# Kernel optimization log

Hardware: AMD Instinct MI355X
Metric: run time of the kernel (lower is better)

The kernel has to match this reference:

```python
import jax, jax.numpy as jnp
import numpy as np


def setup_inputs() -> dict:
    key = jax.random.key(0)
    ks = jax.random.split(key, 7)
    D, N = 32, 3            # directions, ambient dim
    K0, K1, K2 = 500_000, 1_500_000, 1_000_000  # verts, edges, tris
    H = 256                 # num_heights
    return {
        "dirs": jax.random.normal(ks[0], (D, N), jnp.float32),
        "v_coords": jax.random.normal(ks[1], (K0, N), jnp.float32),
        "v_weights": jax.random.uniform(ks[2], (K0,), jnp.float32),
        "edge_verts": jax.random.randint(ks[3], (K1, 2), 0, K0),
        "edge_weights": jax.random.uniform(ks[4], (K1,), jnp.float32),
        "tri_verts": jax.random.randint(ks[5], (K2, 3), 0, K0),
        "tri_weights": jax.random.uniform(ks[6], (K2,), jnp.float32),
        "num_heights": H,
    }


def reference(dirs, v_coords, v_weights, edge_verts, edge_weights,
              tri_verts, tri_weights, num_heights):
    eps = 1e-12
    h = int(num_heights)
    d = dirs.shape[0]
    # L2-normalize directions (torch F.normalize with eps clamp on the norm)
    dirs = dirs / jnp.maximum(jnp.linalg.norm(dirs, axis=1, keepdims=True), eps)

    # vertex height indices: (K0, d)
    v_norms = jnp.linalg.norm(v_coords, axis=1)
    max_height = jnp.maximum(jnp.max(v_norms), eps)
    v_heights = v_coords @ dirs.T
    v_indices = jnp.clip(
        jnp.ceil((h - 1) * (max_height + v_heights) / (2.0 * max_height)),
        0, h - 1,
    ).astype(jnp.int32)

    dir_idx = jnp.arange(d)[None, :]  # broadcast against (k_i, d) bin indices
    diff_wect = jnp.zeros((d, h), jnp.float32)
    # 0-simplices (vertices), sign +1
    diff_wect = diff_wect.at[dir_idx, v_indices].add(v_weights[:, None])
    # 1-simplices (edges), sign (-1)^1 = -1: gather + max over the 2 verts
    edge_bins = jnp.max(v_indices[edge_verts], axis=1)   # (K1, d)
    diff_wect = diff_wect.at[dir_idx, edge_bins].add(-edge_weights[:, None])
    # 2-simplices (triangles), sign (+1): gather + max over the 3 verts
    tri_bins = jnp.max(v_indices[tri_verts], axis=1)     # (K2, d)
    diff_wect = diff_wect.at[dir_idx, tri_bins].add(tri_weights[:, None])

    return jnp.cumsum(diff_wect, axis=1)  # (d, h)
```

## Files before the change

### kernel.cpp

```cpp
#include <hip/hip_runtime.h>
#include <math.h>

#define NDIR 32
#define NH   256
#define BLK  512
#define NB   1024
#define PACKB 256
#define UNIT 64
#define SCALE    2048.0f
#define INVSCALE (1.0 / 2048.0)
#define BIAS  128.5f

#define WS_DIRS 8
#define WS_BMAX 128
#define WS_TAB  512

typedef _Float16 half2v __attribute__((ext_vector_type(2)));

__device__ __forceinline__ unsigned rfl_u(unsigned x) { return __builtin_amdgcn_readfirstlane(x); }

__device__ __forceinline__ unsigned pack2(float x, float y) {
    union { half2v h; unsigned u; } c;
    c.h = half2v{(_Float16)x, (_Float16)y};
    return c.u;
}
__device__ __forceinline__ half2v upk(unsigned u) {
    union { unsigned u; half2v h; } c; c.u = u; return c.h;
}
__device__ __forceinline__ float hdot(half2v a, half2v b, float acc) {
#if __has_builtin(__builtin_amdgcn_fdot2)
    return __builtin_amdgcn_fdot2(a, b, acc, false);
#else
    return acc + (float)a.x * (float)b.x + (float)a.y * (float)b.y;
#endif
}
__device__ __forceinline__ int bin_of(float hs) {
    return (int)fminf(fmaxf(hs, 0.0f), 255.0f);
}

template <bool PACKED>
__global__ void __launch_bounds__(512) wect_prep_kernel(
    const float* __restrict__ dirs, const float* __restrict__ vc, int K0,
    int P, int part_off, float* __restrict__ ws)
{
    int tid  = blockIdx.x * blockDim.x + threadIdx.x;
    int nthr = gridDim.x * blockDim.x;
    for (int i = tid; i < P * NDIR * NH; i += nthr)
        ((int*)ws)[part_off + i] = 0;
    if (blockIdx.x == 0 && threadIdx.x >= 64 && threadIdx.x < 64 + NDIR) {
        int d = threadIdx.x - 64;
        float x = dirs[d * 3 + 0], y = dirs[d * 3 + 1], z = dirs[d * 3 + 2];
        float n = fmaxf(sqrtf(x * x + y * y + z * z), 1e-12f);
        ws[WS_DIRS + d * 3 + 0] = x / n;
        ws[WS_DIRS + d * 3 + 1] = y / n;
        ws[WS_DIRS + d * 3 + 2] = z / n;
    }
    float m = 0.0f;
    uint2* tab = (uint2*)(ws + WS_TAB);
    for (int i = tid; i < K0; i += nthr) {
        float x = vc[3 * i + 0], y = vc[3 * i + 1], z = vc[3 * i + 2];
        m = fmaxf(m, x * x + y * y + z * z);
        if (PACKED) tab[i] = make_uint2(pack2(x, y), pack2(z, 0.0f));
    }
    __shared__ float wm[8];
    #pragma unroll
    for (int off = 32; off > 0; off >>= 1)
        m = fmaxf(m, __shfl_down(m, off, 64));
    if ((threadIdx.x & 63) == 0) wm[threadIdx.x >> 6] = m;
    __syncthreads();
    if (threadIdx.x == 0) {
        float r = wm[0];
        #pragma unroll
        for (int i = 1; i < 8; ++i) r = fmaxf(r, wm[i]);
        ws[WS_BMAX + blockIdx.x] = r;
    }
}

template <bool PACKED>
__global__ void __launch_bounds__(BLK, 8) wect_hist_kernel(
    const float* __restrict__ vc, const float* __restrict__ vw,
    const int*   __restrict__ ev, const float* __restrict__ ew,
    const int*   __restrict__ tv, const float* __restrict__ tw,
    int K0, int K1, int K2, int N0, int N01, int Ntot,
    int P, int part_off, float* __restrict__ ws)
{
    __shared__ int hist[NDIR * NH];
    __shared__ int nctr;
    for (int i = threadIdx.x; i < (NDIR * NH) / 4; i += BLK)
        ((int4*)hist)[i] = make_int4(0, 0, 0, 0);

    const int wave = threadIdx.x >> 6;
    const int lane = threadIdx.x & 63;
    const int b    = blockIdx.x;
    const int nu   = (Ntot - b + NB - 1) / NB;
    if (threadIdx.x == 0) nctr = 8;

    float m = 0.0f;
    for (int i = lane; i < PACKB; i += 64) m = fmaxf(m, ws[WS_BMAX + i]);
    #pragma unroll
    for (int off = 32; off > 0; off >>= 1)
        m = fmaxf(m, __shfl_xor(m, off, 64));
    float maxh = fmaxf(sqrtf(m), 1e-12f);
    float inv  = 127.5f / maxh;

    unsigned sdxy[NDIR], sdz[NDIR];
    #pragma unroll
    for (int d = 0; d < NDIR; ++d) {
        float dx = ws[WS_DIRS + 3 * d + 0] * inv;
        float dy = ws[WS_DIRS + 3 * d + 1] * inv;
        float dz = ws[WS_DIRS + 3 * d + 2] * inv;
        sdxy[d] = rfl_u(pack2(dx, dy));
        sdz[d]  = rfl_u(pack2(dz, 0.0f));
    }
    __syncthreads();

    const uint2* tab = (const uint2*)(ws + WS_TAB);
    #define LDC(J, CXY, CZ)                                                  \
        do {                                                                 \
            if constexpr (PACKED) {                                          \
                uint2 r = tab[J];                                            \
                CXY = upk(r.x); CZ = upk(r.y);                               \
            } else {                                                         \
                float _x = vc[3 * (J) + 0], _y = vc[3 * (J) + 1], _z = vc[3 * (J) + 2]; \
                CXY = half2v{(_Float16)_x, (_Float16)_y};                    \
                CZ  = half2v{(_Float16)_z, (_Float16)0.0f};                  \
            }                                                                \
        } while (0)

    int n = wave;
    while (n < nu) {
        int nxt = 0;
        if (lane == 0) nxt = atomicAdd(&nctr, 1);
        const int u = b + n * NB;

        if (u < N0) {
            int i = u * UNIT + lane;
            int j = (i < K0) ? i : 0;
            half2v xy, z;
            LDC(j, xy, z);
            int w = (i < K0) ? __float2int_rn(vw[j] * SCALE) : 0;
            #pragma unroll
            for (int d = 0; d < NDIR; ++d) {
                half2v dxy = upk(sdxy[d]), dz = upk(sdz[d]);
                float h = hdot(xy, dxy, hdot(z, dz, BIAS));
                atomicAdd(&hist[d * NH + bin_of(h)], w);
            }
        } else if (u < N01) {
            int i = (u - N0) * UNIT + lane;
            int j = (i < K1) ? i : 0;
            int2 e = ((const int2*)ev)[j];
            half2v axy, az, bxy, bz;
            LDC(e.x, axy, az);
            LDC(e.y, bxy, bz);
            int w = (i < K1) ? -__float2int_rn(ew[j] * SCALE) : 0;
            #pragma unroll
            for (int d = 0; d < NDIR; ++d) {
                half2v dxy = upk(sdxy[d]), dz = upk(sdz[d]);
                float h = fmaxf(hdot(axy, dxy, hdot(az, dz, BIAS)),
                                hdot(bxy, dxy, hdot(bz, dz, BIAS)));
                atomicAdd(&hist[d * NH + bin_of(h)], w);
            }
        } else {
            int i = (u - N01) * UNIT + lane;
            int j = (i < K2) ? i : 0;
            int va = tv[3 * j + 0], vb = tv[3 * j + 1], vcc = tv[3 * j + 2];
            half2v axy, az, bxy, bz, cxy, cz;
            LDC(va,  axy, az);
            LDC(vb,  bxy, bz);
            LDC(vcc, cxy, cz);
            int w = (i < K2) ? __float2int_rn(tw[j] * SCALE) : 0;
            #pragma unroll
            for (int d = 0; d < NDIR; ++d) {
                half2v dxy = upk(sdxy[d]), dz = upk(sdz[d]);
                float h = fmaxf(fmaxf(hdot(axy, dxy, hdot(az, dz, BIAS)),
                                      hdot(bxy, dxy, hdot(bz, dz, BIAS))),
                                hdot(cxy, dxy, hdot(cz, dz, BIAS)));
                atomicAdd(&hist[d * NH + bin_of(h)], w);
            }
        }

        n = __shfl(nxt, 0, 64);
    }
    #undef LDC

    __syncthreads();
    int* part = (int*)ws + part_off + (blockIdx.x & (P - 1)) * (NDIR * NH);
    for (int i = threadIdx.x; i < NDIR * NH; i += BLK) {
        int v = hist[i];
        if (v != 0) atomicAdd(&part[i], v);
    }
}

__global__ void wect_reduce_kernel(const float* __restrict__ ws, int P, int part_off,
                                   float* __restrict__ out) {
    __shared__ long long s[NH];
    int d = blockIdx.x, h = threadIdx.x;
    const int* part = (const int*)ws + part_off + d * NH + h;
    long long acc = 0;
    #pragma unroll 4
    for (int p = 0; p < P; ++p)
        acc += (long long)part[p * (NDIR * NH)];
    s[h] = acc;
    __syncthreads();
    #pragma unroll
    for (int off = 1; off < NH; off <<= 1) {
        long long v = (h >= off) ? s[h - off] : 0;
        __syncthreads();
        s[h] += v;
        __syncthreads();
    }
    out[d * NH + h] = (float)((double)s[h] * INVSCALE);
}

extern "C" void kernel_launch(void* const* d_in, const int* in_sizes, int n_in,
                              void* d_out, int out_size, void* d_ws, size_t ws_size,
                              hipStream_t stream) {
    const float* dirs = (const float*)d_in[0];
    const float* vc   = (const float*)d_in[1];
    const float* vw   = (const float*)d_in[2];
    const int*   ev   = (const int*)d_in[3];
    const float* ew   = (const float*)d_in[4];
    const int*   tv   = (const int*)d_in[5];
    const float* tw   = (const float*)d_in[6];
    int K0 = in_sizes[2];
    int K1 = in_sizes[4];
    int K2 = in_sizes[6];

    float* ws  = (float*)d_ws;
    float* out = (float*)d_out;

    long long words = (long long)(ws_size / 4);

    int  part_off = WS_TAB + 2 * K0;
    bool packed   = (words - part_off) >= 8LL * NDIR * NH;
    if (!packed) part_off = WS_TAB;

    long long availP = (words - part_off) / (NDIR * NH);
    int P = 1;
    while (P * 2 <= availP && P < 16) P *= 2;

    int N0 = (K0 + UNIT - 1) / UNIT;
    int N1 = (K1 + UNIT - 1) / UNIT;
    int N2 = (K2 + UNIT - 1) / UNIT;
    int N01 = N0 + N1;
    int Ntot = N01 + N2;

    if (packed) {
        wect_prep_kernel<true><<<PACKB, 512, 0, stream>>>(dirs, vc, K0, P, part_off, ws);
        wect_hist_kernel<true><<<NB, BLK, 0, stream>>>(
            vc, vw, ev, ew, tv, tw, K0, K1, K2, N0, N01, Ntot, P, part_off, ws);
    } else {
        wect_prep_kernel<false><<<PACKB, 512, 0, stream>>>(dirs, vc, K0, P, part_off, ws);
        wect_hist_kernel<false><<<NB, BLK, 0, stream>>>(
            vc, vw, ev, ew, tv, tw, K0, K1, K2, N0, N01, Ntot, P, part_off, ws);
    }
    wect_reduce_kernel<<<NDIR, NH, 0, stream>>>(ws, P, part_off, out);
}
```

Before: 62.10 us.

## Software-pipeline index loads and vertex gathers ahead of histogram compute

Restructures the work-stealing loop into a three-stage software pipeline with two register stages (A and B). Each iteration loads simplex indices two units ahead and gathers packed vertex coordinates and weights one unit ahead while it runs the binning and LDS atomics for the current unit. The aim is to hide global-memory gather latency behind the atomic-heavy compute. In exchange it uses more registers, which may reduce occupancy. Vertices and edges now always do three gathers, with duplicate indices standing in for the missing vertices, which adds redundant loads.

```diff
diff --git a/kernel.cpp b/kernel.cpp
--- a/kernel.cpp
+++ b/kernel.cpp
@@ -115,73 +115,119 @@
     __syncthreads();
 
     const uint2* tab = (const uint2*)(ws + WS_TAB);
-    #define LDC(J, CXY, CZ)                                                  \
-        do {                                                                 \
-            if constexpr (PACKED) {                                          \
-                uint2 r = tab[J];                                            \
-                CXY = upk(r.x); CZ = upk(r.y);                               \
-            } else {                                                         \
-                float _x = vc[3 * (J) + 0], _y = vc[3 * (J) + 1], _z = vc[3 * (J) + 2]; \
-                CXY = half2v{(_Float16)_x, (_Float16)_y};                    \
-                CZ  = half2v{(_Float16)_z, (_Float16)0.0f};                  \
-            }                                                                \
+
+    int ia_A, ib_A, ic_A, ia_B, ib_B, ic_B;
+    float wf_A = 0.0f, wf_B = 0.0f;
+    half2v axy_A{}, az_A{}, bxy_A{}, bz_A{}, cxy_A{}, cz_A{};
+    half2v axy_B{}, az_B{}, bxy_B{}, bz_B{}, cxy_B{}, cz_B{};
+    ia_A = ib_A = ic_A = ia_B = ib_B = ic_B = 0;
+
+    #define STAGE_IDX(U, S)                                                   \
+        do { int u_ = (U);                                                    \
+            if (u_ < N0) {                                                    \
+                int i_ = u_ * UNIT + lane;                                    \
+                int j_ = (i_ < K0) ? i_ : 0;                                  \
+                ia_##S = j_; ib_##S = j_; ic_##S = j_;                        \
+            } else if (u_ < N01) {                                            \
+                int i_ = (u_ - N0) * UNIT + lane;                             \
+                int j_ = (i_ < K1) ? i_ : 0;                                  \
+                int2 e_ = ((const int2*)ev)[j_];                              \
+                ia_##S = e_.x; ib_##S = e_.y; ic_##S = e_.y;                  \
+            } else {                                                          \
+                int i_ = (u_ - N01) * UNIT + lane;                            \
+                int j_ = (i_ < K2) ? i_ : 0;                                  \
+                ia_##S = tv[3 * j_ + 0];                                      \
+                ib_##S = tv[3 * j_ + 1];                                      \
+                ic_##S = tv[3 * j_ + 2];                                      \
+            }                                                                 \
         } while (0)
 
-    int n = wave;
-    while (n < nu) {
-        int nxt = 0;
-        if (lane == 0) nxt = atomicAdd(&nctr, 1);
-        const int u = b + n * NB;
-
-        if (u < N0) {
-            int i = u * UNIT + lane;
-            int j = (i < K0) ? i : 0;
-            half2v xy, z;
-            LDC(j, xy, z);
-            int w = (i < K0) ? __float2int_rn(vw[j] * SCALE) : 0;
-            #pragma unroll
-            for (int d = 0; d < NDIR; ++d) {
-                half2v dxy = upk(sdxy[d]), dz = upk(sdz[d]);
-                float h = hdot(xy, dxy, hdot(z, dz, BIAS));
-                atomicAdd(&hist[d * NH + bin_of(h)], w);
-            }
-        } else if (u < N01) {
-            int i = (u - N0) * UNIT + lane;
-            int j = (i < K1) ? i : 0;
-            int2 e = ((const int2*)ev)[j];
-            half2v axy, az, bxy, bz;
-            LDC(e.x, axy, az);
-            LDC(e.y, bxy, bz);
-            int w = (i < K1) ? -__float2int_rn(ew[j] * SCALE) : 0;
-            #pragma unroll
-            for (int d = 0; d < NDIR; ++d) {
-                half2v dxy = upk(sdxy[d]), dz = upk(sdz[d]);
-                float h = fmaxf(hdot(axy, dxy, hdot(az, dz, BIAS)),
-                                hdot(bxy, dxy, hdot(bz, dz, BIAS)));
-                atomicAdd(&hist[d * NH + bin_of(h)], w);
-            }
-        } else {
-            int i = (u - N01) * UNIT + lane;
-            int j = (i < K2) ? i : 0;
-            int va = tv[3 * j + 0], vb = tv[3 * j + 1], vcc = tv[3 * j + 2];
-            half2v axy, az, bxy, bz, cxy, cz;
-            LDC(va,  axy, az);
-            LDC(vb,  bxy, bz);
-            LDC(vcc, cxy, cz);
-            int w = (i < K2) ? __float2int_rn(tw[j] * SCALE) : 0;
-            #pragma unroll
-            for (int d = 0; d < NDIR; ++d) {
-                half2v dxy = upk(sdxy[d]), dz = upk(sdz[d]);
-                float h = fmaxf(fmaxf(hdot(axy, dxy, hdot(az, dz, BIAS)),
-                                      hdot(bxy, dxy, hdot(bz, dz, BIAS))),
-                                hdot(cxy, dxy, hdot(cz, dz, BIAS)));
-                atomicAdd(&hist[d * NH + bin_of(h)], w);
-            }
-        }
-
-        n = __shfl(nxt, 0, 64);
-    }
-    #undef LDC
+    #define STAGE_GATHER(U, S)                                                \
+        do { int u_ = (U);                                                    \
+            if constexpr (PACKED) {                                           \
+                uint2 ra_ = tab[ia_##S], rb_ = tab[ib_##S], rc_ = tab[ic_##S];\
+                axy_##S = upk(ra_.x); az_##S = upk(ra_.y);                    \
+                bxy_##S = upk(rb_.x); bz_##S = upk(rb_.y);                    \
+                cxy_##S = upk(rc_.x); cz_##S = upk(rc_.y);                    \
+            } else {                                                          \
+                float ax_ = vc[3 * ia_##S], ay_ = vc[3 * ia_##S + 1], azv_ = vc[3 * ia_##S + 2]; \
+                float bx_ = vc[3 * ib_##S], by_ = vc[3 * ib_##S + 1], bzv_ = vc[3 * ib_##S + 2]; \
+                float cx_ = vc[3 * ic_##S], cy_ = vc[3 * ic_##S + 1], czv_ = vc[3 * ic_##S + 2]; \
+                axy_##S = half2v{(_Float16)ax_, (_Float16)ay_}; az_##S = half2v{(_Float16)azv_, (_Float16)0.0f}; \
+                bxy_##S = half2v{(_Float16)bx_, (_Float16)by_}; bz_##S = half2v{(_Float16)bzv_, (_Float16)0.0f}; \
+                cxy_##S = half2v{(_Float16)cx_, (_Float16)cy_}; cz_##S = half2v{(_Float16)czv_, (_Float16)0.0f}; \
+            }                                                                 \
+            if (u_ < N0) {                                                    \
+                int i_ = u_ * UNIT + lane;                                    \
+                wf_##S = (i_ < K0) ? vw[i_] : 0.0f;                           \
+            } else if (u_ < N01) {                                            \
+                int i_ = (u_ - N0) * UNIT + lane;                             \
+                wf_##S = (i_ < K1) ? -ew[i_] : 0.0f;                          \
+            } else {                                                          \
+                int i_ = (u_ - N01) * UNIT + lane;                            \
+                wf_##S = (i_ < K2) ? tw[i_] : 0.0f;                           \
+            }                                                                 \
+        } while (0)
+
+    #define STAGE_COMPUTE(U, S)                                               \
+        do { int u_ = (U);                                                    \
+            int w_ = __float2int_rn(wf_##S * SCALE);                          \
+            if (u_ < N0) {                                                    \
+                _Pragma("unroll")                                             \
+                for (int d = 0; d < NDIR; ++d) {                              \
+                    half2v dxy = upk(sdxy[d]), dz = upk(sdz[d]);              \
+                    float h = hdot(axy_##S, dxy, hdot(az_##S, dz, BIAS));     \
+                    atomicAdd(&hist[d * NH + bin_of(h)], w_);                 \
+                }                                                             \
+            } else if (u_ < N01) {                                            \
+                _Pragma("unroll")                                             \
+                for (int d = 0; d < NDIR; ++d) {                              \
+                    half2v dxy = upk(sdxy[d]), dz = upk(sdz[d]);              \
+                    float h = fmaxf(hdot(axy_##S, dxy, hdot(az_##S, dz, BIAS)), \
+                                    hdot(bxy_##S, dxy, hdot(bz_##S, dz, BIAS))); \
+                    atomicAdd(&hist[d * NH + bin_of(h)], w_);                 \
+                }                                                             \
+            } else {                                                          \
+                _Pragma("unroll")                                             \
+                for (int d = 0; d < NDIR; ++d) {                              \
+                    half2v dxy = upk(sdxy[d]), dz = upk(sdz[d]);              \
+                    float h = fmaxf(fmaxf(hdot(axy_##S, dxy, hdot(az_##S, dz, BIAS)), \
+                                          hdot(bxy_##S, dxy, hdot(bz_##S, dz, BIAS))), \
+                                    hdot(cxy_##S, dxy, hdot(cz_##S, dz, BIAS))); \
+                    atomicAdd(&hist[d * NH + bin_of(h)], w_);                 \
+                }                                                             \
+            }                                                                 \
+        } while (0)
+
+    int t = 0;
+    if (lane == 0) t = atomicAdd(&nctr, 1);
+    int n1 = __shfl(t, 0, 64);
+    if (lane == 0) t = atomicAdd(&nctr, 1);
+    int n2 = __shfl(t, 0, 64);
+    int n0 = wave, n3;
+
+    if (n0 < nu) STAGE_IDX(b + n0 * NB, A);
+    if (n1 < nu) STAGE_IDX(b + n1 * NB, B);
+    if (n0 < nu) STAGE_GATHER(b + n0 * NB, A);
+
+    while (n0 < nu) {
+        if (n2 < nu) STAGE_IDX(b + n2 * NB, A);
+        if (n1 < nu) STAGE_GATHER(b + n1 * NB, B);
+        if (lane == 0) t = atomicAdd(&nctr, 1);
+        STAGE_COMPUTE(b + n0 * NB, A);
+        n3 = __shfl(t, 0, 64);
+        n0 = n1; n1 = n2; n2 = n3;
+        if (n0 >= nu) break;
+        if (n2 < nu) STAGE_IDX(b + n2 * NB, B);
+        if (n1 < nu) STAGE_GATHER(b + n1 * NB, A);
+        if (lane == 0) t = atomicAdd(&nctr, 1);
+        STAGE_COMPUTE(b + n0 * NB, B);
+        n3 = __shfl(t, 0, 64);
+        n0 = n1; n1 = n2; n2 = n3;
+    }
+    #undef STAGE_IDX
+    #undef STAGE_GATHER
+    #undef STAGE_COMPUTE
 
     __syncthreads();
     int* part = (int*)ws + part_off + (blockIdx.x & (P - 1)) * (NDIR * NH);
```

Result: slower. 187.6 us (+202.0%).

## Software-pipeline histogram gathers with double buffering and lookahead work stealing

Applied to the files above, without the earlier changes.

Replaces the single work-stealing loop with three per-simplex-type loops. Each wave claims units two steps ahead and double-buffers vertex gathers and weights. For edges and triangles it also fetches the next unit's vertex indices one stage earlier, so the dependent coordinate gathers overlap the current unit's 32-direction LDS atomic loop. This aims to hide global gather latency, at the cost of more live registers and more code, which may lower occupancy under the launch bounds.

```diff
diff --git a/kernel.cpp b/kernel.cpp
--- a/kernel.cpp
+++ b/kernel.cpp
@@ -18,6 +18,7 @@
 typedef _Float16 half2v __attribute__((ext_vector_type(2)));
 
 __device__ __forceinline__ unsigned rfl_u(unsigned x) { return __builtin_amdgcn_readfirstlane(x); }
+__device__ __forceinline__ int      rfl_i(int x)      { return __builtin_amdgcn_readfirstlane(x); }
 
 __device__ __forceinline__ unsigned pack2(float x, float y) {
     union { half2v h; unsigned u; } c;
@@ -93,6 +94,8 @@
     const int lane = threadIdx.x & 63;
     const int b    = blockIdx.x;
     const int nu   = (Ntot - b + NB - 1) / NB;
+    const int e0   = (N0  > b) ? (N0  - b + NB - 1) / NB : 0;
+    const int e1   = (N01 > b) ? (N01 - b + NB - 1) / NB : 0;
     if (threadIdx.x == 0) nctr = 8;
 
     float m = 0.0f;
@@ -115,73 +118,149 @@
     __syncthreads();
 
     const uint2* tab = (const uint2*)(ws + WS_TAB);
-    #define LDC(J, CXY, CZ)                                                  \
-        do {                                                                 \
-            if constexpr (PACKED) {                                          \
-                uint2 r = tab[J];                                            \
-                CXY = upk(r.x); CZ = upk(r.y);                               \
-            } else {                                                         \
-                float _x = vc[3 * (J) + 0], _y = vc[3 * (J) + 1], _z = vc[3 * (J) + 2]; \
-                CXY = half2v{(_Float16)_x, (_Float16)_y};                    \
-                CZ  = half2v{(_Float16)_z, (_Float16)0.0f};                  \
-            }                                                                \
+    #define LROW(J, XY, Z)                                                    \
+        do {                                                                  \
+            if constexpr (PACKED) {                                           \
+                uint2 r_ = tab[J]; XY = upk(r_.x); Z = upk(r_.y);             \
+            } else {                                                          \
+                float x_ = vc[3 * (J)], y_ = vc[3 * (J) + 1], z_ = vc[3 * (J) + 2]; \
+                XY = half2v{(_Float16)x_, (_Float16)y_};                      \
+                Z  = half2v{(_Float16)z_, (_Float16)0.0f};                    \
+            }                                                                 \
         } while (0)
 
-    int n = wave;
-    while (n < nu) {
-        int nxt = 0;
-        if (lane == 0) nxt = atomicAdd(&nctr, 1);
-        const int u = b + n * NB;
-
-        if (u < N0) {
-            int i = u * UNIT + lane;
-            int j = (i < K0) ? i : 0;
-            half2v xy, z;
-            LDC(j, xy, z);
-            int w = (i < K0) ? __float2int_rn(vw[j] * SCALE) : 0;
-            #pragma unroll
-            for (int d = 0; d < NDIR; ++d) {
-                half2v dxy = upk(sdxy[d]), dz = upk(sdz[d]);
-                float h = hdot(xy, dxy, hdot(z, dz, BIAS));
-                atomicAdd(&hist[d * NH + bin_of(h)], w);
-            }
-        } else if (u < N01) {
-            int i = (u - N0) * UNIT + lane;
-            int j = (i < K1) ? i : 0;
-            int2 e = ((const int2*)ev)[j];
-            half2v axy, az, bxy, bz;
-            LDC(e.x, axy, az);
-            LDC(e.y, bxy, bz);
-            int w = (i < K1) ? -__float2int_rn(ew[j] * SCALE) : 0;
-            #pragma unroll
-            for (int d = 0; d < NDIR; ++d) {
-                half2v dxy = upk(sdxy[d]), dz = upk(sdz[d]);
-                float h = fmaxf(hdot(axy, dxy, hdot(az, dz, BIAS)),
-                                hdot(bxy, dxy, hdot(bz, dz, BIAS)));
-                atomicAdd(&hist[d * NH + bin_of(h)], w);
-            }
-        } else {
-            int i = (u - N01) * UNIT + lane;
-            int j = (i < K2) ? i : 0;
-            int va = tv[3 * j + 0], vb = tv[3 * j + 1], vcc = tv[3 * j + 2];
-            half2v axy, az, bxy, bz, cxy, cz;
-            LDC(va,  axy, az);
-            LDC(vb,  bxy, bz);
-            LDC(vcc, cxy, cz);
-            int w = (i < K2) ? __float2int_rn(tw[j] * SCALE) : 0;
-            #pragma unroll
-            for (int d = 0; d < NDIR; ++d) {
-                half2v dxy = upk(sdxy[d]), dz = upk(sdz[d]);
-                float h = fmaxf(fmaxf(hdot(axy, dxy, hdot(az, dz, BIAS)),
-                                      hdot(bxy, dxy, hdot(bz, dz, BIAS))),
-                                hdot(cxy, dxy, hdot(cz, dz, BIAS)));
-                atomicAdd(&hist[d * NH + bin_of(h)], w);
-            }
+    #define STEAL() do { if (lane == 0) t = atomicAdd(&nctr, 1); } while (0)
+
+    int t = 0, n0 = wave, n1, n2;
+    STEAL(); n1 = rfl_i(t);
+    STEAL(); n2 = rfl_i(t);
+
+    {
+        half2v xyA{}, zA{}, xyB{}, zB{};
+        float wA = 0.0f, wB = 0.0f;
+        #define VGATH(N, S)                                                   \
+            do { int i_ = (b + (N) * NB) * UNIT + lane;                       \
+                 int j_ = (i_ < K0) ? i_ : 0;                                 \
+                 LROW(j_, xy##S, z##S);                                       \
+                 w##S = (i_ < K0) ? vw[j_] : 0.0f; } while (0)
+        #define VCOMP(S)                                                      \
+            do { int wi_ = __float2int_rn(w##S * SCALE);                      \
+                 _Pragma("unroll")                                            \
+                 for (int d = 0; d < NDIR; ++d) {                             \
+                     half2v dxy = upk(sdxy[d]), dz = upk(sdz[d]);             \
+                     float h = hdot(xy##S, dxy, hdot(z##S, dz, BIAS));        \
+                     atomicAdd(&hist[d * NH + bin_of(h)], wi_);               \
+                 } } while (0)
+        if (n0 < e0) VGATH(n0, A);
+        while (n0 < e0) {
+            if (n1 < e0) VGATH(n1, B);
+            STEAL();
+            VCOMP(A);
+            n0 = n1; n1 = n2; n2 = rfl_i(t);
+            if (n0 >= e0) break;
+            if (n1 < e0) VGATH(n1, A);
+            STEAL();
+            VCOMP(B);
+            n0 = n1; n1 = n2; n2 = rfl_i(t);
         }
-
-        n = __shfl(nxt, 0, 64);
-    }
-    #undef LDC
+        #undef VGATH
+        #undef VCOMP
+    }
+
+    {
+        int iaA = 0, ibA = 0, iaB = 0, ibB = 0;
+        half2v axyA{}, azA{}, bxyA{}, bzA{};
+        half2v axyB{}, azB{}, bxyB{}, bzB{};
+        float wA = 0.0f, wB = 0.0f;
+        #define EIDX(N, S)                                                    \
+            do { int i_ = (b + (N) * NB - N0) * UNIT + lane;                  \
+                 int j_ = (i_ < K1) ? i_ : 0;                                 \
+                 int2 e_ = ((const int2*)ev)[j_];                             \
+                 ia##S = e_.x; ib##S = e_.y; } while (0)
+        #define EGATH(N, S)                                                   \
+            do { LROW(ia##S, axy##S, az##S);                                  \
+                 LROW(ib##S, bxy##S, bz##S);                                  \
+                 int i_ = (b + (N) * NB - N0) * UNIT + lane;                  \
+                 w##S = (i_ < K1) ? -ew[i_] : 0.0f; } while (0)
+        #define ECOMP(S)                                                      \
+            do { int wi_ = __float2int_rn(w##S * SCALE);                      \
+                 _Pragma("unroll")                                            \
+                 for (int d = 0; d < NDIR; ++d) {                             \
+                     half2v dxy = upk(sdxy[d]), dz = upk(sdz[d]);             \
+                     float h = fmaxf(hdot(axy##S, dxy, hdot(az##S, dz, BIAS)),\
+                                     hdot(bxy##S, dxy, hdot(bz##S, dz, BIAS)));\
+                     atomicAdd(&hist[d * NH + bin_of(h)], wi_);               \
+                 } } while (0)
+        if (n0 < e1) EIDX(n0, A);
+        if (n1 < e1) EIDX(n1, B);
+        if (n0 < e1) EGATH(n0, A);
+        while (n0 < e1) {
+            if (n1 < e1) EGATH(n1, B);
+            if (n2 < e1) EIDX(n2, A);
+            STEAL();
+            ECOMP(A);
+            n0 = n1; n1 = n2; n2 = rfl_i(t);
+            if (n0 >= e1) break;
+            if (n1 < e1) EGATH(n1, A);
+            if (n2 < e1) EIDX(n2, B);
+            STEAL();
+            ECOMP(B);
+            n0 = n1; n1 = n2; n2 = rfl_i(t);
+        }
+        #undef EIDX
+        #undef EGATH
+        #undef ECOMP
+    }
+
+    {
+        int iaA = 0, ibA = 0, icA = 0, iaB = 0, ibB = 0, icB = 0;
+        half2v axyA{}, azA{}, bxyA{}, bzA{}, cxyA{}, czA{};
+        half2v axyB{}, azB{}, bxyB{}, bzB{}, cxyB{}, czB{};
+        float wA = 0.0f, wB = 0.0f;
+        #define TIDX(N, S)                                                    \
+            do { int i_ = (b + (N) * NB - N01) * UNIT + lane;                 \
+                 int j_ = (i_ < K2) ? i_ : 0;                                 \
+                 ia##S = tv[3 * j_ + 0];                                      \
+                 ib##S = tv[3 * j_ + 1];                                      \
+                 ic##S = tv[3 * j_ + 2]; } while (0)
+        #define TGATH(N, S)                                                   \
+            do { LROW(ia##S, axy##S, az##S);                                  \
+                 LROW(ib##S, bxy##S, bz##S);                                  \
+                 LROW(ic##S, cxy##S, cz##S);                                  \
+                 int i_ = (b + (N) * NB - N01) * UNIT + lane;                 \
+                 w##S = (i_ < K2) ? tw[i_] : 0.0f; } while (0)
+        #define TCOMP(S)                                                      \
+            do { int wi_ = __float2int_rn(w##S * SCALE);                      \
+                 _Pragma("unroll")                                            \
+                 for (int d = 0; d < NDIR; ++d) {                             \
+                     half2v dxy = upk(sdxy[d]), dz = upk(sdz[d]);             \
+                     float h = fmaxf(fmaxf(hdot(axy##S, dxy, hdot(az##S, dz, BIAS)),  \
+                                           hdot(bxy##S, dxy, hdot(bz##S, dz, BIAS))), \
+                                     hdot(cxy##S, dxy, hdot(cz##S, dz, BIAS)));\
+                     atomicAdd(&hist[d * NH + bin_of(h)], wi_);               \
+                 } } while (0)
+        if (n0 < nu) TIDX(n0, A);
+        if (n1 < nu) TIDX(n1, B);
+        if (n0 < nu) TGATH(n0, A);
+        while (n0 < nu) {
+            if (n1 < nu) TGATH(n1, B);
+            if (n2 < nu) TIDX(n2, A);
+            STEAL();
+            TCOMP(A);
+            n0 = n1; n1 = n2; n2 = rfl_i(t);
+            if (n0 >= nu) break;
+            if (n1 < nu) TGATH(n1, A);
+            if (n2 < nu) TIDX(n2, B);
+            STEAL();
+            TCOMP(B);
+            n0 = n1; n1 = n2; n2 = rfl_i(t);
+        }
+        #undef TIDX
+        #undef TGATH
+        #undef TCOMP
+    }
+    #undef LROW
+    #undef STEAL
 
     __syncthreads();
     int* part = (int*)ws + part_off + (blockIdx.x & (P - 1)) * (NDIR * NH);
```

After: 65.93 us. +6.2%, slower.

## Replace packed fp16 dot products with fp32 FMAs and LDS-broadcast directions

Applied to the files above, without the earlier changes.

Swaps the packed-half fdot2 height computation for plain fp32 FMAs, with the scaled directions kept in a shared float4 array that wave 0 fills, instead of 64 SGPR-resident packed constants recomputed by every wave. It also clamps bins with fmed3 and broadcasts the next work index with readfirstlane instead of a shuffle. This trades the dot instruction count (now 3 FMAs per vertex per direction instead of 2 dot2) plus LDS broadcast reads for less scalar register pressure and cheaper prologue work. The fp32 heights may also shift bin assignment slightly compared with the fp16 path.

```diff
diff --git a/kernel.cpp b/kernel.cpp
--- a/kernel.cpp
+++ b/kernel.cpp
@@ -17,7 +17,7 @@
 
 typedef _Float16 half2v __attribute__((ext_vector_type(2)));
 
-__device__ __forceinline__ unsigned rfl_u(unsigned x) { return __builtin_amdgcn_readfirstlane(x); }
+__device__ __forceinline__ int rfl_i(int x) { return __builtin_amdgcn_readfirstlane(x); }
 
 __device__ __forceinline__ unsigned pack2(float x, float y) {
     union { half2v h; unsigned u; } c;
@@ -27,15 +27,12 @@
 __device__ __forceinline__ half2v upk(unsigned u) {
     union { unsigned u; half2v h; } c; c.u = u; return c.h;
 }
-__device__ __forceinline__ float hdot(half2v a, half2v b, float acc) {
-#if __has_builtin(__builtin_amdgcn_fdot2)
-    return __builtin_amdgcn_fdot2(a, b, acc, false);
+__device__ __forceinline__ int bin_of(float hs) {
+#if __has_builtin(__builtin_amdgcn_fmed3f)
+    return (int)__builtin_amdgcn_fmed3f(hs, 0.0f, 255.0f);
 #else
-    return acc + (float)a.x * (float)b.x + (float)a.y * (float)b.y;
+    return (int)fminf(fmaxf(hs, 0.0f), 255.0f);
 #endif
-}
-__device__ __forceinline__ int bin_of(float hs) {
-    return (int)fminf(fmaxf(hs, 0.0f), 255.0f);
 }
 
 template <bool PACKED>
@@ -85,6 +82,7 @@
     int P, int part_off, float* __restrict__ ws)
 {
     __shared__ int hist[NDIR * NH];
+    __shared__ float4 sdirs[NDIR];
     __shared__ int nctr;
     for (int i = threadIdx.x; i < (NDIR * NH) / 4; i += BLK)
         ((int4*)hist)[i] = make_int4(0, 0, 0, 0);
@@ -95,36 +93,32 @@
     const int nu   = (Ntot - b + NB - 1) / NB;
     if (threadIdx.x == 0) nctr = 8;
 
-    float m = 0.0f;
-    for (int i = lane; i < PACKB; i += 64) m = fmaxf(m, ws[WS_BMAX + i]);
-    #pragma unroll
-    for (int off = 32; off > 0; off >>= 1)
-        m = fmaxf(m, __shfl_xor(m, off, 64));
-    float maxh = fmaxf(sqrtf(m), 1e-12f);
-    float inv  = 127.5f / maxh;
-
-    unsigned sdxy[NDIR], sdz[NDIR];
-    #pragma unroll
-    for (int d = 0; d < NDIR; ++d) {
-        float dx = ws[WS_DIRS + 3 * d + 0] * inv;
-        float dy = ws[WS_DIRS + 3 * d + 1] * inv;
-        float dz = ws[WS_DIRS + 3 * d + 2] * inv;
-        sdxy[d] = rfl_u(pack2(dx, dy));
-        sdz[d]  = rfl_u(pack2(dz, 0.0f));
+    if (wave == 0) {
+        float m = 0.0f;
+        for (int i = lane; i < PACKB; i += 64) m = fmaxf(m, ws[WS_BMAX + i]);
+        #pragma unroll
+        for (int off = 32; off > 0; off >>= 1)
+            m = fmaxf(m, __shfl_xor(m, off, 64));
+        float maxh = fmaxf(sqrtf(m), 1e-12f);
+        float inv  = 127.5f / maxh;
+        if (lane < NDIR) {
+            sdirs[lane] = make_float4(ws[WS_DIRS + 3 * lane + 0] * inv,
+                                      ws[WS_DIRS + 3 * lane + 1] * inv,
+                                      ws[WS_DIRS + 3 * lane + 2] * inv, 0.0f);
+        }
     }
     __syncthreads();
 
     const uint2* tab = (const uint2*)(ws + WS_TAB);
-    #define LDC(J, CXY, CZ)                                                  \
-        do {                                                                 \
-            if constexpr (PACKED) {                                          \
-                uint2 r = tab[J];                                            \
-                CXY = upk(r.x); CZ = upk(r.y);                               \
-            } else {                                                         \
-                float _x = vc[3 * (J) + 0], _y = vc[3 * (J) + 1], _z = vc[3 * (J) + 2]; \
-                CXY = half2v{(_Float16)_x, (_Float16)_y};                    \
-                CZ  = half2v{(_Float16)_z, (_Float16)0.0f};                  \
-            }                                                                \
+    #define LDC3(J, X, Y, Z)                                                  \
+        do {                                                                  \
+            if constexpr (PACKED) {                                           \
+                uint2 r_ = tab[J];                                            \
+                half2v p_ = upk(r_.x), q_ = upk(r_.y);                        \
+                X = (float)p_.x; Y = (float)p_.y; Z = (float)q_.x;            \
+            } else {                                                          \
+                X = vc[3 * (J) + 0]; Y = vc[3 * (J) + 1]; Z = vc[3 * (J) + 2];\
+            }                                                                 \
         } while (0)
 
     int n = wave;
@@ -136,52 +130,54 @@
         if (u < N0) {
             int i = u * UNIT + lane;
             int j = (i < K0) ? i : 0;
-            half2v xy, z;
-            LDC(j, xy, z);
+            float x, y, z;
+            LDC3(j, x, y, z);
             int w = (i < K0) ? __float2int_rn(vw[j] * SCALE) : 0;
             #pragma unroll
             for (int d = 0; d < NDIR; ++d) {
-                half2v dxy = upk(sdxy[d]), dz = upk(sdz[d]);
-                float h = hdot(xy, dxy, hdot(z, dz, BIAS));
+                float4 D = sdirs[d];
+                float h = fmaf(x, D.x, fmaf(y, D.y, fmaf(z, D.z, BIAS)));
                 atomicAdd(&hist[d * NH + bin_of(h)], w);
             }
         } else if (u < N01) {
             int i = (u - N0) * UNIT + lane;
             int j = (i < K1) ? i : 0;
             int2 e = ((const int2*)ev)[j];
-            half2v axy, az, bxy, bz;
-            LDC(e.x, axy, az);
-            LDC(e.y, bxy, bz);
+            float ax, ay, az, bx, by, bz;
+            LDC3(e.x, ax, ay, az);
+            LDC3(e.y, bx, by, bz);
             int w = (i < K1) ? -__float2int_rn(ew[j] * SCALE) : 0;
             #pragma unroll
             for (int d = 0; d < NDIR; ++d) {
-                half2v dxy = upk(sdxy[d]), dz = upk(sdz[d]);
-                float h = fmaxf(hdot(axy, dxy, hdot(az, dz, BIAS)),
-                                hdot(bxy, dxy, hdot(bz, dz, BIAS)));
+                float4 D = sdirs[d];
+                float ha = fmaf(ax, D.x, fmaf(ay, D.y, fmaf(az, D.z, BIAS)));
+                float hb = fmaf(bx, D.x, fmaf(by, D.y, fmaf(bz, D.z, BIAS)));
+                float h  = fmaxf(ha, hb);
                 atomicAdd(&hist[d * NH + bin_of(h)], w);
             }
         } else {
             int i = (u - N01) * UNIT + lane;
             int j = (i < K2) ? i : 0;
             int va = tv[3 * j + 0], vb = tv[3 * j + 1], vcc = tv[3 * j + 2];
-            half2v axy, az, bxy, bz, cxy, cz;
-            LDC(va,  axy, az);
-            LDC(vb,  bxy, bz);
-            LDC(vcc, cxy, cz);
+            float ax, ay, az, bx, by, bz, cx, cy, cz;
+            LDC3(va,  ax, ay, az);
+            LDC3(vb,  bx, by, bz);
+            LDC3(vcc, cx, cy, cz);
             int w = (i < K2) ? __float2int_rn(tw[j] * SCALE) : 0;
             #pragma unroll
             for (int d = 0; d < NDIR; ++d) {
-                half2v dxy = upk(sdxy[d]), dz = upk(sdz[d]);
-                float h = fmaxf(fmaxf(hdot(axy, dxy, hdot(az, dz, BIAS)),
-                                      hdot(bxy, dxy, hdot(bz, dz, BIAS))),
-                                hdot(cxy, dxy, hdot(cz, dz, BIAS)));
+                float4 D = sdirs[d];
+                float ha = fmaf(ax, D.x, fmaf(ay, D.y, fmaf(az, D.z, BIAS)));
+                float hb = fmaf(bx, D.x, fmaf(by, D.y, fmaf(bz, D.z, BIAS)));
+                float hc = fmaf(cx, D.x, fmaf(cy, D.y, fmaf(cz, D.z, BIAS)));
+                float h  = fmaxf(fmaxf(ha, hb), hc);
                 atomicAdd(&hist[d * NH + bin_of(h)], w);
             }
         }
 
-        n = __shfl(nxt, 0, 64);
-    }
-    #undef LDC
+        n = rfl_i(nxt);
+    }
+    #undef LDC3
 
     __syncthreads();
     int* part = (int*)ws + part_off + (blockIdx.x & (P - 1)) * (NDIR * NH);
```

Result: slower. 75.43 us (+21.5%).
